# Optimization experiments

Measured on AMD Instinct MI355X. Metric: run time of the kernel, lower is better.

## Reference

```python
import jax, jax.numpy as jnp
import numpy as np

DIM = 2048

def setup_inputs() -> dict:
    key = jax.random.key(0)
    k_x, k_q, k_k, k_v, k_o = jax.random.split(key, 5)
    scale = 1.0 / np.sqrt(DIM)
    x = jax.random.normal(k_x, (2, 4096, DIM), dtype=jnp.float32)
    # nn.Linear weights are [out, in]; y = x @ W^T
    wq = jax.random.normal(k_q, (DIM, DIM), dtype=jnp.float32) * scale
    wk = jax.random.normal(k_k, (DIM, DIM), dtype=jnp.float32) * scale
    wv = jax.random.normal(k_v, (DIM, DIM), dtype=jnp.float32) * scale
    wo = jax.random.normal(k_o, (DIM, DIM), dtype=jnp.float32) * scale
    return {"x": x, "wq": wq, "wk": wk, "wv": wv, "wo": wo}

def reference(x, wq, wk, wv, wo):
    # Faithful to the torch module: NO head split; full-dim QK^T, scale by sqrt(dim).
    q = jnp.einsum('bsd,ed->bse', x, wq)
    k = jnp.einsum('bsd,ed->bse', x, wk)
    v = jnp.einsum('bsd,ed->bse', x, wv)
    scores = jnp.einsum('bqd,bkd->bqk', q, k) / jnp.sqrt(jnp.asarray(DIM, x.dtype))
    attn = jax.nn.softmax(scores, axis=-1)
    ctx = jnp.einsum('bqk,bkd->bqd', attn, v)
    return jnp.einsum('bsd,ed->bse', ctx, wo)
```

## Files before the change

### kernel.cpp

```cpp
#include <hip/hip_runtime.h>
#include <hip/hip_bf16.h>
#include <stdint.h>
#include <math.h>

typedef __attribute__((ext_vector_type(4))) float f32x4;
typedef __attribute__((ext_vector_type(8))) short s16x8;

typedef const __attribute__((address_space(1))) void* gas_ptr;
typedef __attribute__((address_space(3))) void* las_ptr;

__device__ __forceinline__ float bf2f(unsigned short u) {
    union { unsigned int i; float f; } x; x.i = ((unsigned int)u) << 16; return x.f;
}
__device__ __forceinline__ unsigned short f2bf(float f) {
    union { float f; unsigned int u; } x; x.f = f;
    unsigned int r = x.u + 0x7FFFu + ((x.u >> 16) & 1u);
    return (unsigned short)(r >> 16);
}

__global__ __launch_bounds__(256) void cvt_f32_bf16(const float* __restrict__ src,
                                                    unsigned short* __restrict__ dst,
                                                    long n) {
    long i = ((long)blockIdx.x * 256 + threadIdx.x) * 8;
    if (i + 8 > n) return;
    f32x4 a = *(const f32x4*)(src + i);
    f32x4 b = *(const f32x4*)(src + i + 4);
    s16x8 o;
    o[0] = (short)f2bf(a[0]); o[1] = (short)f2bf(a[1]);
    o[2] = (short)f2bf(a[2]); o[3] = (short)f2bf(a[3]);
    o[4] = (short)f2bf(b[0]); o[5] = (short)f2bf(b[1]);
    o[6] = (short)f2bf(b[2]); o[7] = (short)f2bf(b[3]);
    *(s16x8*)(dst + i) = o;
}

template <typename CT>
__global__ __launch_bounds__(512, 2)
void gemm256_bt(const unsigned short* __restrict__ A,
                const unsigned short* __restrict__ B,
                CT* __restrict__ C,
                int N, int K, int nt,
                long sA, long sB, long sC, float alpha)
{
    A += (long)blockIdx.z * sA;
    B += (long)blockIdx.z * sB;
    C += (long)blockIdx.z * sC;

    __shared__ unsigned short L[2][2][2][128][64];

    const int t    = threadIdx.x;
    const int lane = t & 63;
    const int wid  = t >> 6;
    const int wm   = wid >> 2;
    const int wn   = wid & 3;
    const long brow = (long)blockIdx.x * 256;
    const long bcol = (long)blockIdx.y * 256;

    const int lr = lane & 15;
    const int hi = lane >> 4;
    const int sw = (lr & 7) << 3;

    int voff[2];
    const unsigned short* pA[2][2];
    const unsigned short* pB[2][2];
    {
        const unsigned short* Ab = A + brow * K;
        const unsigned short* Bb = B + bcol * K;
        #pragma unroll
        for (int j = 0; j < 2; ++j) {
            int u  = t + 512 * j;
            int ix = u >> 3;
            int cg = u & 7;
            int cs = (cg * 8) ^ ((ix & 7) << 3);
            voff[j] = u * 8;
            long ra0 = ((long)(ix >> 6) << 7) | (0 << 6) | (ix & 63);
            long ra1 = ((long)(ix >> 6) << 7) | (1 << 6) | (ix & 63);
            long rb0 = ((long)(ix >> 5) << 6) | (0 << 5) | (ix & 31);
            long rb1 = ((long)(ix >> 5) << 6) | (1 << 5) | (ix & 31);
            pA[0][j] = Ab + ra0 * K + cs;
            pA[1][j] = Ab + ra1 * K + cs;
            pB[0][j] = Bb + rb0 * K + cs;
            pB[1][j] = Bb + rb1 * K + cs;
        }
    }

#define STAGE_A(H, KT) do { \
    _Pragma("unroll") \
    for (int j = 0; j < 2; ++j) \
        __builtin_amdgcn_global_load_lds((gas_ptr)(pA[H][j] + (long)(KT) * 64), \
            (las_ptr)(&L[(KT) & 1][0][H][0][0] + voff[j]), 16, 0, 0); \
} while (0)
#define STAGE_B(H, KT) do { \
    _Pragma("unroll") \
    for (int j = 0; j < 2; ++j) \
        __builtin_amdgcn_global_load_lds((gas_ptr)(pB[H][j] + (long)(KT) * 64), \
            (las_ptr)(&L[(KT) & 1][1][H][0][0] + voff[j]), 16, 0, 0); \
} while (0)

#define LOAD_AF(QM) do { \
    _Pragma("unroll") \
    for (int m = 0; m < 4; ++m) \
        _Pragma("unroll") \
        for (int kk = 0; kk < 2; ++kk) \
            af[m][kk] = *(const s16x8*)&L[cur][0][QM][wm * 64 + m * 16 + lr][(kk * 32 + hi * 8) ^ sw]; \
} while (0)
#define LOAD_BQ(DST, QN) do { \
    _Pragma("unroll") \
    for (int n = 0; n < 2; ++n) \
        _Pragma("unroll") \
        for (int kk = 0; kk < 2; ++kk) \
            DST[n][kk] = *(const s16x8*)&L[cur][1][QN][wn * 32 + n * 16 + lr][(kk * 32 + hi * 8) ^ sw]; \
} while (0)
#define MFMA_Q(QM, QN, BQ) do { \
    __builtin_amdgcn_s_setprio(1); \
    _Pragma("unroll") \
    for (int m = 0; m < 4; ++m) \
        _Pragma("unroll") \
        for (int n = 0; n < 2; ++n) \
            _Pragma("unroll") \
            for (int kk = 0; kk < 2; ++kk) \
                acc[(QM) * 4 + m][(QN) * 2 + n] = __builtin_amdgcn_mfma_f32_16x16x32_bf16( \
                    af[m][kk], BQ[n][kk], acc[(QM) * 4 + m][(QN) * 2 + n], 0, 0, 0); \
    __builtin_amdgcn_s_setprio(0); \
} while (0)

    f32x4 acc[8][4];
    #pragma unroll
    for (int m = 0; m < 8; ++m)
        #pragma unroll
        for (int n = 0; n < 4; ++n)
            acc[m][n] = {0.f, 0.f, 0.f, 0.f};

    STAGE_A(0, 0); STAGE_A(1, 0); STAGE_B(0, 0); STAGE_B(1, 0);
    if (nt > 1) {
        STAGE_A(0, 1); STAGE_B(0, 1);
        asm volatile("s_waitcnt vmcnt(4)" ::: "memory");
    } else {
        asm volatile("s_waitcnt vmcnt(0)" ::: "memory");
    }
    __builtin_amdgcn_s_barrier();

    for (int kt = 0; kt < nt; ++kt) {
        const int cur = kt & 1;
        s16x8 af[4][2], bq0[2][2], bq1[2][2];

        LOAD_AF(0);
        LOAD_BQ(bq0, 0);
        if (kt + 1 < nt) STAGE_A(1, kt + 1);
        asm volatile("s_waitcnt lgkmcnt(8)" ::: "memory");
        __builtin_amdgcn_s_barrier();
        asm volatile("s_waitcnt lgkmcnt(0)" ::: "memory");
        MFMA_Q(0, 0, bq0);
        __builtin_amdgcn_s_barrier();

        LOAD_BQ(bq1, 1);
        if (kt + 1 < nt) STAGE_B(1, kt + 1);
        __builtin_amdgcn_s_barrier();
        asm volatile("s_waitcnt lgkmcnt(0)" ::: "memory");
        MFMA_Q(0, 1, bq1);
        __builtin_amdgcn_s_barrier();

        LOAD_AF(1);
        if (kt + 2 < nt) STAGE_A(0, kt + 2);
        asm volatile("s_waitcnt lgkmcnt(4)" ::: "memory");
        __builtin_amdgcn_s_barrier();
        asm volatile("s_waitcnt lgkmcnt(0)" ::: "memory");
        MFMA_Q(1, 1, bq1);
        __builtin_amdgcn_s_barrier();

        if (kt + 2 < nt) STAGE_B(0, kt + 2);
        __builtin_amdgcn_s_barrier();
        MFMA_Q(1, 0, bq0);

        if (kt + 1 < nt) {
            if (kt + 2 < nt) asm volatile("s_waitcnt vmcnt(4)" ::: "memory");
            else             asm volatile("s_waitcnt vmcnt(0)" ::: "memory");
            __builtin_amdgcn_s_barrier();
        }
    }
#undef STAGE_A
#undef STAGE_B
#undef LOAD_AF
#undef LOAD_BQ
#undef MFMA_Q

    #pragma unroll
    for (int m = 0; m < 8; ++m) {
        #pragma unroll
        for (int n = 0; n < 4; ++n) {
            #pragma unroll
            for (int i = 0; i < 4; ++i) {
                long row = brow + wm * 128 + m * 16 + hi * 4 + i;
                long col = bcol + wn * 64 + n * 16 + lr;
                float vv = acc[m][n][i] * alpha;
                if constexpr (sizeof(CT) == 2) {
                    ((unsigned short*)C)[row * (long)N + col] = f2bf(vv);
                } else {
                    ((float*)C)[row * (long)N + col] = vv;
                }
            }
        }
    }
}

__global__ __launch_bounds__(256) void transpose_bf16(const unsigned short* __restrict__ src,
                                                      unsigned short* __restrict__ dst,
                                                      int srows, int scols) {
    __shared__ unsigned short tile[64][66];
    const long bofs = (long)blockIdx.z * srows * scols;
    const unsigned short* s = src + bofs;
    unsigned short* d = dst + bofs;
    const int c0 = blockIdx.x * 64;
    const int r0 = blockIdx.y * 64;
    const int tx = threadIdx.x & 15;
    const int ty = threadIdx.x >> 4;

    #pragma unroll
    for (int k = 0; k < 4; ++k) {
        int r = ty + 16 * k;
        ushort4 v = *(const ushort4*)(s + (long)(r0 + r) * scols + c0 + tx * 4);
        tile[r][tx * 4 + 0] = v.x; tile[r][tx * 4 + 1] = v.y;
        tile[r][tx * 4 + 2] = v.z; tile[r][tx * 4 + 3] = v.w;
    }
    __syncthreads();
    #pragma unroll
    for (int k = 0; k < 4; ++k) {
        int dr = ty + 16 * k;
        ushort4 v;
        v.x = tile[tx * 4 + 0][dr]; v.y = tile[tx * 4 + 1][dr];
        v.z = tile[tx * 4 + 2][dr]; v.w = tile[tx * 4 + 3][dr];
        *(ushort4*)(d + (long)(c0 + dr) * srows + r0 + tx * 4) = v;
    }
}

__global__ __launch_bounds__(256) void softmax_inplace(unsigned short* __restrict__ S, int ncols) {
    const long row = blockIdx.x;
    unsigned short* p = S + row * (long)ncols;
    const int t = threadIdx.x;
    const int wid = t >> 6;

    ushort4 raw[4];
    const ushort4* pv = (const ushort4*)(p + t * 16);
    #pragma unroll
    for (int i = 0; i < 4; ++i) raw[i] = pv[i];

    float v[16];
    float mx = -1e30f;
    #pragma unroll
    for (int i = 0; i < 4; ++i) {
        v[4*i+0] = bf2f(raw[i].x); v[4*i+1] = bf2f(raw[i].y);
        v[4*i+2] = bf2f(raw[i].z); v[4*i+3] = bf2f(raw[i].w);
    }
    #pragma unroll
    for (int i = 0; i < 16; ++i) mx = fmaxf(mx, v[i]);
    #pragma unroll
    for (int off = 32; off > 0; off >>= 1) mx = fmaxf(mx, __shfl_xor(mx, off));

    __shared__ float red[8];
    if ((t & 63) == 0) red[wid] = mx;
    __syncthreads();
    mx = fmaxf(fmaxf(red[0], red[1]), fmaxf(red[2], red[3]));

    float sum = 0.f;
    #pragma unroll
    for (int i = 0; i < 16; ++i) { v[i] = __expf(v[i] - mx); sum += v[i]; }
    #pragma unroll
    for (int off = 32; off > 0; off >>= 1) sum += __shfl_xor(sum, off);
    __syncthreads();
    if ((t & 63) == 0) red[4 + wid] = sum;
    __syncthreads();
    sum = red[4] + red[5] + red[6] + red[7];
    const float inv = 1.0f / sum;

    ushort4* po = (ushort4*)(p + t * 16);
    #pragma unroll
    for (int i = 0; i < 4; ++i) {
        ushort4 o;
        o.x = f2bf(v[4*i+0] * inv); o.y = f2bf(v[4*i+1] * inv);
        o.z = f2bf(v[4*i+2] * inv); o.w = f2bf(v[4*i+3] * inv);
        po[i] = o;
    }
}

extern "C" void kernel_launch(void* const* d_in, const int* in_sizes, int n_in,
                              void* d_out, int out_size, void* d_ws, size_t ws_size,
                              hipStream_t stream) {
    const float* x  = (const float*)d_in[0];
    const float* wq = (const float*)d_in[1];
    const float* wk = (const float*)d_in[2];
    const float* wv = (const float*)d_in[3];
    const float* wo = (const float*)d_in[4];
    float* out = (float*)d_out;

    const long SDIM = 2048, SEQ = 4096, BATCH = 2;
    const long MS = BATCH * SEQ;
    const long XN = MS * SDIM;
    const long WN = SDIM * SDIM;

    unsigned short* ws  = (unsigned short*)d_ws;
    unsigned short* Xbf = ws;
    unsigned short* Wqb = ws + XN;
    unsigned short* Wkb = Wqb + WN;
    unsigned short* Wvb = Wkb + WN;
    unsigned short* Wob = Wvb + WN;
    unsigned short* Qb  = Wob + WN;
    unsigned short* Kb  = Qb + XN;
    unsigned short* Vb  = Kb + XN;
    unsigned short* Sb  = Vb + XN;
    unsigned short* Vt  = Xbf;
    unsigned short* Ctx = Qb;

    cvt_f32_bf16<<<(int)(XN / 2048), 256, 0, stream>>>(x,  Xbf, XN);
    cvt_f32_bf16<<<(int)(WN / 2048), 256, 0, stream>>>(wq, Wqb, WN);
    cvt_f32_bf16<<<(int)(WN / 2048), 256, 0, stream>>>(wk, Wkb, WN);
    cvt_f32_bf16<<<(int)(WN / 2048), 256, 0, stream>>>(wv, Wvb, WN);
    cvt_f32_bf16<<<(int)(WN / 2048), 256, 0, stream>>>(wo, Wob, WN);

    dim3 gp((unsigned)(MS / 256), (unsigned)(SDIM / 256), 1);
    gemm256_bt<unsigned short><<<gp, 512, 0, stream>>>(Xbf, Wqb, Qb, (int)SDIM, (int)SDIM, (int)(SDIM / 64), 0, 0, 0, 1.0f);
    gemm256_bt<unsigned short><<<gp, 512, 0, stream>>>(Xbf, Wkb, Kb, (int)SDIM, (int)SDIM, (int)(SDIM / 64), 0, 0, 0, 1.0f);
    gemm256_bt<unsigned short><<<gp, 512, 0, stream>>>(Xbf, Wvb, Vb, (int)SDIM, (int)SDIM, (int)(SDIM / 64), 0, 0, 0, 1.0f);

    dim3 gt((unsigned)(SDIM / 64), (unsigned)(SEQ / 64), (unsigned)BATCH);
    transpose_bf16<<<gt, 256, 0, stream>>>(Vb, Vt, (int)SEQ, (int)SDIM);

    const float scale = 1.0f / sqrtf((float)SDIM);
    dim3 gs((unsigned)(SEQ / 256), (unsigned)(SEQ / 256), (unsigned)BATCH);
    gemm256_bt<unsigned short><<<gs, 512, 0, stream>>>(Qb, Kb, Sb, (int)SEQ, (int)SDIM, (int)(SDIM / 64),
                                                       SEQ * SDIM, SEQ * SDIM, SEQ * SEQ, scale);

    softmax_inplace<<<(int)(BATCH * SEQ), 256, 0, stream>>>(Sb, (int)SEQ);

    dim3 gc((unsigned)(SEQ / 256), (unsigned)(SDIM / 256), (unsigned)BATCH);
    gemm256_bt<unsigned short><<<gc, 512, 0, stream>>>(Sb, Vt, Ctx, (int)SDIM, (int)SEQ, (int)(SEQ / 64),
                                                       SEQ * SEQ, SDIM * SEQ, SEQ * SDIM, 1.0f);

    gemm256_bt<float><<<gp, 512, 0, stream>>>(Ctx, Wob, out, (int)SDIM, (int)SDIM, (int)(SDIM / 64), 0, 0, 0, 1.0f);
}
```

Measured before the change: 583.3 us.

## Prefetch next-tile LDS fragments during MFMA and unroll k-loop by two

Restructures the GEMM main loop so the register fragments for the next k-tile (A sub-tile 0 and B sub-tile 0) are read from LDS while the current tile's last MFMA quadrants run. The A fragments are double-buffered in registers (afA/afB), and the loop is unrolled by two so the LDS buffer index is a compile-time constant. sched_barrier calls pin the instruction order. The goal is to hide LDS read latency behind MFMA work, at the cost of more VGPRs and extra barriers/waitcnts that must be exactly correct. The new code assumes nt is even and at least 2, and it drops the nt>1 guard in the prologue.

```diff
diff --git a/kernel.cpp b/kernel.cpp
--- a/kernel.cpp
+++ b/kernel.cpp
@@ -83,34 +83,34 @@
         }
     }
 
-#define STAGE_A(H, KT) do { \
+#define STAGE_A(H, KT, BUF) do { \
     _Pragma("unroll") \
     for (int j = 0; j < 2; ++j) \
         __builtin_amdgcn_global_load_lds((gas_ptr)(pA[H][j] + (long)(KT) * 64), \
-            (las_ptr)(&L[(KT) & 1][0][H][0][0] + voff[j]), 16, 0, 0); \
-} while (0)
-#define STAGE_B(H, KT) do { \
+            (las_ptr)(&L[BUF][0][H][0][0] + voff[j]), 16, 0, 0); \
+} while (0)
+#define STAGE_B(H, KT, BUF) do { \
     _Pragma("unroll") \
     for (int j = 0; j < 2; ++j) \
         __builtin_amdgcn_global_load_lds((gas_ptr)(pB[H][j] + (long)(KT) * 64), \
-            (las_ptr)(&L[(KT) & 1][1][H][0][0] + voff[j]), 16, 0, 0); \
-} while (0)
-
-#define LOAD_AF(QM) do { \
+            (las_ptr)(&L[BUF][1][H][0][0] + voff[j]), 16, 0, 0); \
+} while (0)
+
+#define LOAD_A(DST, BUF, SUB) do { \
     _Pragma("unroll") \
     for (int m = 0; m < 4; ++m) \
         _Pragma("unroll") \
         for (int kk = 0; kk < 2; ++kk) \
-            af[m][kk] = *(const s16x8*)&L[cur][0][QM][wm * 64 + m * 16 + lr][(kk * 32 + hi * 8) ^ sw]; \
-} while (0)
-#define LOAD_BQ(DST, QN) do { \
+            DST[m][kk] = *(const s16x8*)&L[BUF][0][SUB][wm * 64 + m * 16 + lr][(kk * 32 + hi * 8) ^ sw]; \
+} while (0)
+#define LOAD_B(DST, BUF, SUB) do { \
     _Pragma("unroll") \
     for (int n = 0; n < 2; ++n) \
         _Pragma("unroll") \
         for (int kk = 0; kk < 2; ++kk) \
-            DST[n][kk] = *(const s16x8*)&L[cur][1][QN][wn * 32 + n * 16 + lr][(kk * 32 + hi * 8) ^ sw]; \
-} while (0)
-#define MFMA_Q(QM, QN, BQ) do { \
+            DST[n][kk] = *(const s16x8*)&L[BUF][1][SUB][wn * 32 + n * 16 + lr][(kk * 32 + hi * 8) ^ sw]; \
+} while (0)
+#define MFMA_Q(QM, QN, AF, BQ) do { \
     __builtin_amdgcn_s_setprio(1); \
     _Pragma("unroll") \
     for (int m = 0; m < 4; ++m) \
@@ -119,7 +119,7 @@
             _Pragma("unroll") \
             for (int kk = 0; kk < 2; ++kk) \
                 acc[(QM) * 4 + m][(QN) * 2 + n] = __builtin_amdgcn_mfma_f32_16x16x32_bf16( \
-                    af[m][kk], BQ[n][kk], acc[(QM) * 4 + m][(QN) * 2 + n], 0, 0, 0); \
+                    AF[m][kk], BQ[n][kk], acc[(QM) * 4 + m][(QN) * 2 + n], 0, 0, 0); \
     __builtin_amdgcn_s_setprio(0); \
 } while (0)
 
@@ -130,57 +130,65 @@
         for (int n = 0; n < 4; ++n)
             acc[m][n] = {0.f, 0.f, 0.f, 0.f};
 
-    STAGE_A(0, 0); STAGE_A(1, 0); STAGE_B(0, 0); STAGE_B(1, 0);
-    if (nt > 1) {
-        STAGE_A(0, 1); STAGE_B(0, 1);
-        asm volatile("s_waitcnt vmcnt(4)" ::: "memory");
-    } else {
-        asm volatile("s_waitcnt vmcnt(0)" ::: "memory");
-    }
+    s16x8 afA[4][2], afB[4][2], bq0[2][2], bq1[2][2];
+
+    STAGE_A(0, 0, 0); STAGE_B(0, 0, 0); STAGE_A(1, 0, 0); STAGE_B(1, 0, 0);
+    STAGE_A(0, 1, 1); STAGE_B(0, 1, 1);
+    asm volatile("s_waitcnt vmcnt(8)" ::: "memory");
     __builtin_amdgcn_s_barrier();
-
-    for (int kt = 0; kt < nt; ++kt) {
-        const int cur = kt & 1;
-        s16x8 af[4][2], bq0[2][2], bq1[2][2];
-
-        LOAD_AF(0);
-        LOAD_BQ(bq0, 0);
-        if (kt + 1 < nt) STAGE_A(1, kt + 1);
-        asm volatile("s_waitcnt lgkmcnt(8)" ::: "memory");
-        __builtin_amdgcn_s_barrier();
-        asm volatile("s_waitcnt lgkmcnt(0)" ::: "memory");
-        MFMA_Q(0, 0, bq0);
-        __builtin_amdgcn_s_barrier();
-
-        LOAD_BQ(bq1, 1);
-        if (kt + 1 < nt) STAGE_B(1, kt + 1);
-        __builtin_amdgcn_s_barrier();
-        asm volatile("s_waitcnt lgkmcnt(0)" ::: "memory");
-        MFMA_Q(0, 1, bq1);
-        __builtin_amdgcn_s_barrier();
-
-        LOAD_AF(1);
-        if (kt + 2 < nt) STAGE_A(0, kt + 2);
-        asm volatile("s_waitcnt lgkmcnt(4)" ::: "memory");
-        __builtin_amdgcn_s_barrier();
-        asm volatile("s_waitcnt lgkmcnt(0)" ::: "memory");
-        MFMA_Q(1, 1, bq1);
-        __builtin_amdgcn_s_barrier();
-
-        if (kt + 2 < nt) STAGE_B(0, kt + 2);
-        __builtin_amdgcn_s_barrier();
-        MFMA_Q(1, 0, bq0);
-
-        if (kt + 1 < nt) {
-            if (kt + 2 < nt) asm volatile("s_waitcnt vmcnt(4)" ::: "memory");
-            else             asm volatile("s_waitcnt vmcnt(0)" ::: "memory");
-            __builtin_amdgcn_s_barrier();
-        }
-    }
+    LOAD_A(afA, 0, 0);
+    LOAD_B(bq0, 0, 0);
+    asm volatile("s_waitcnt vmcnt(4)" ::: "memory");
+    __builtin_amdgcn_s_barrier();
+
+#define TILE(CUR, KTE) do { \
+    const int kt_ = (KTE); \
+     \
+    LOAD_B(bq1, CUR, 1); \
+    if (kt_ + 1 < nt) STAGE_A(1, kt_ + 1, CUR ^ 1); \
+    __builtin_amdgcn_s_barrier(); \
+    asm volatile("s_waitcnt lgkmcnt(4)" ::: "memory"); \
+    __builtin_amdgcn_sched_barrier(0); \
+    MFMA_Q(0, 0, afA, bq0); \
+    __builtin_amdgcn_s_barrier(); \
+     \
+    LOAD_A(afB, CUR, 1); \
+    if (kt_ + 1 < nt) STAGE_B(1, kt_ + 1, CUR ^ 1); \
+    __builtin_amdgcn_s_barrier(); \
+    asm volatile("s_waitcnt lgkmcnt(8)" ::: "memory"); \
+    __builtin_amdgcn_sched_barrier(0); \
+    MFMA_Q(0, 1, afA, bq1); \
+    asm volatile("s_waitcnt vmcnt(4)" ::: "memory"); \
+    __builtin_amdgcn_s_barrier(); \
+     \
+    if (kt_ + 1 < nt) { \
+        LOAD_A(afA, CUR ^ 1, 0); \
+        if (kt_ + 2 < nt) STAGE_A(0, kt_ + 2, CUR); \
+    } \
+    __builtin_amdgcn_s_barrier(); \
+    if (kt_ + 1 < nt) { asm volatile("s_waitcnt lgkmcnt(8)" ::: "memory"); } \
+    else              { asm volatile("s_waitcnt lgkmcnt(0)" ::: "memory"); } \
+    __builtin_amdgcn_sched_barrier(0); \
+    MFMA_Q(1, 1, afB, bq1); \
+    __builtin_amdgcn_s_barrier(); \
+     \
+    if (kt_ + 2 < nt) STAGE_B(0, kt_ + 2, CUR); \
+    __builtin_amdgcn_s_barrier(); \
+    MFMA_Q(1, 0, afB, bq0); \
+    if (kt_ + 1 < nt) LOAD_B(bq0, CUR ^ 1, 0); \
+    asm volatile("s_waitcnt vmcnt(4)" ::: "memory"); \
+    __builtin_amdgcn_s_barrier(); \
+} while (0)
+
+    for (int kt = 0; kt < nt; kt += 2) {
+        TILE(0, kt);
+        TILE(1, kt + 1);
+    }
+#undef TILE
 #undef STAGE_A
 #undef STAGE_B
-#undef LOAD_AF
-#undef LOAD_BQ
+#undef LOAD_A
+#undef LOAD_B
 #undef MFMA_Q
 
     #pragma unroll
```

Measured after the change: 848.0 us. 1.45x slower.
